# Optimization experiments

Hardware: AMD Instinct MI355X
Metric: run time of the kernel (lower is better)

## Reference

```python
import jax, jax.numpy as jnp
import numpy as np

B, N, F_IN, D_OUT, EMB_DIM = 4, 2048, 64, 128, 16
H1, D1 = 4, D_OUT // 4   # gat1: 4 heads, 32 per head
H2, D2 = 1, D_OUT        # gat2: 1 head, 128
NEG_INF = -1e9
LN_EPS = 1e-3  # keras LayerNormalization default epsilon


def setup_inputs() -> dict:
    key = jax.random.key(0)
    ks = jax.random.split(key, 12)
    def glorot(k, shape):
        lim = np.sqrt(6.0 / (shape[0] + shape[1]))
        return jax.random.uniform(k, shape, jnp.float32, -lim, lim)
    return {
        "x": jax.random.normal(ks[0], (B, N, F_IN), jnp.float32),
        "emb": glorot(ks[1], (N, EMB_DIM)),
        "q1_w": glorot(ks[2], (F_IN, H1 * D1)), "q1_b": jnp.zeros((H1 * D1,), jnp.float32),
        "k1_w": glorot(ks[3], (F_IN, H1 * D1)), "k1_b": jnp.zeros((H1 * D1,), jnp.float32),
        "v1_w": glorot(ks[4], (F_IN, H1 * D1)), "v1_b": jnp.zeros((H1 * D1,), jnp.float32),
        "q2_w": glorot(ks[5], (D_OUT, H2 * D2)), "q2_b": jnp.zeros((H2 * D2,), jnp.float32),
        "k2_w": glorot(ks[6], (D_OUT, H2 * D2)), "k2_b": jnp.zeros((H2 * D2,), jnp.float32),
        "v2_w": glorot(ks[7], (D_OUT, H2 * D2)), "v2_b": jnp.zeros((H2 * D2,), jnp.float32),
        "proj_w": glorot(ks[8], (F_IN, D_OUT)),
        "ln_g": jnp.ones((D_OUT,), jnp.float32),
        "ln_b": jnp.zeros((D_OUT,), jnp.float32),
    }


def _adaptive_adj(emb):
    # tf.math.l2_normalize(axis=-1, epsilon=1e-12)
    sq = jnp.maximum(jnp.sum(emb * emb, axis=-1, keepdims=True), 1e-12)
    n = emb * jax.lax.rsqrt(sq)
    adj = jax.nn.sigmoid(n @ n.T)
    eye = jnp.eye(N, dtype=jnp.float32)
    return adj + eye - adj * eye  # force diag to 1


def _graph_attention(x, adj, qw, qb, kw, kb, vw, vb, heads, d):
    b, n, _ = x.shape
    q = (x @ qw + qb).reshape(b, n, heads, d)
    k = (x @ kw + kb).reshape(b, n, heads, d)
    v = (x @ vw + vb).reshape(b, n, heads, d)
    scores = jnp.einsum('bihd,bjhd->bhij', q, k) / jnp.sqrt(jnp.float32(d))
    scores = jnp.where(adj[None, None] == 0, NEG_INF, scores)
    w = jax.nn.softmax(scores, axis=-1)  # dropout inactive (training=False)
    out = jnp.einsum('bhij,bjhd->bihd', w, v)
    return out.reshape(b, n, heads * d)


def reference(x, emb, q1_w, q1_b, k1_w, k1_b, v1_w, v1_b,
              q2_w, q2_b, k2_w, k2_b, v2_w, v2_b, proj_w, ln_g, ln_b):
    input_projected = x @ proj_w
    adj = _adaptive_adj(emb)
    h = _graph_attention(x, adj, q1_w, q1_b, k1_w, k1_b, v1_w, v1_b, H1, D1)
    h = jax.nn.relu(h)
    h = _graph_attention(h, adj, q2_w, q2_b, k2_w, k2_b, v2_w, v2_b, H2, D2)
    y = h + input_projected
    mu = jnp.mean(y, axis=-1, keepdims=True)
    var = jnp.mean((y - mu) ** 2, axis=-1, keepdims=True)
    return (y - mu) * jax.lax.rsqrt(var + LN_EPS) * ln_g + ln_b
```

## Files before the change

kernel.cpp:

```cpp
#include <hip/hip_runtime.h>
#include <hip/hip_bf16.h>

#define NB 4
#define NN 2048
#define FIN 64
#define DOUT 128

typedef __hip_bfloat16 bf16;
typedef __attribute__((ext_vector_type(8))) short short8;
typedef __attribute__((ext_vector_type(4))) float f32x4;
typedef __attribute__((ext_vector_type(4))) int int4v;

static __device__ __forceinline__ float bf2f(bf16 v) { return __bfloat162float(v); }
static __device__ __forceinline__ bf16  f2bf(float v) { return __float2bfloat16(v); }
static __device__ __forceinline__ unsigned bfbits(float v) {
    bf16 h = __float2bfloat16(v);
    return (unsigned)*reinterpret_cast<unsigned short*>(&h);
}


__global__ __launch_bounds__(256) void k_gemm1(
    const float* __restrict__ x,
    const float* __restrict__ q1w, const float* __restrict__ q1b,
    const float* __restrict__ k1w, const float* __restrict__ k1b,
    const float* __restrict__ v1w, const float* __restrict__ v1b,
    const float* __restrict__ pw,
    bf16* __restrict__ qA, bf16* __restrict__ kA, bf16* __restrict__ vT,
    float* __restrict__ proj)
{
    __shared__ float At[64][65];
    __shared__ float Wt[64][65];
    const int rb = blockIdx.x;
    const int cb = blockIdx.y;
    const int mat = cb >> 1;
    const int c0 = (cb & 1) * 64;
    const float* W    = (mat==0)? q1w : (mat==1)? k1w : (mat==2)? v1w : pw;
    const float* bias = (mat==0)? q1b : (mat==1)? k1b : (mat==2)? v1b : nullptr;
    const int t = threadIdx.x;
    const int row0 = rb * 64;
    for (int e = t; e < 1024; e += 256) {
        int r = e >> 4, c4 = e & 15;
        *(float4*)&At[r][c4*4] = *(const float4*)&x[(size_t)(row0 + r)*FIN + c4*4];
        *(float4*)&Wt[r][c4*4] = *(const float4*)&W[(size_t)r*DOUT + c0 + c4*4];
    }
    __syncthreads();
    const int ty = t >> 4, tx = t & 15;
    float acc[4][4] = {};
    #pragma unroll 8
    for (int k = 0; k < 64; ++k) {
        float av[4], bv[4];
        #pragma unroll
        for (int i = 0; i < 4; ++i) av[i] = At[ty*4+i][k];
        #pragma unroll
        for (int j = 0; j < 4; ++j) bv[j] = Wt[k][tx*4+j];
        #pragma unroll
        for (int i = 0; i < 4; ++i)
            #pragma unroll
            for (int j = 0; j < 4; ++j)
                acc[i][j] = fmaf(av[i], bv[j], acc[i][j]);
    }
    #pragma unroll
    for (int i = 0; i < 4; ++i) {
        int gr = row0 + ty*4 + i;
        int b = gr >> 11, n = gr & 2047;
        #pragma unroll
        for (int j = 0; j < 4; ++j) {
            int gc = c0 + tx*4 + j;
            float v = acc[i][j] + (bias ? bias[gc] : 0.f);
            if (mat == 3) { proj[(size_t)gr*DOUT + gc] = v; continue; }
            int hd = gc >> 5, d32 = gc & 31;
            if (mat == 2) {
                int kt = n >> 6, ks2 = (n >> 5) & 1, q4k = (n >> 3) & 3, jk = n & 7;
                int mt = d32 >> 4, n16d = d32 & 15;
                size_t idx = ((((size_t)(b*4+hd)*32 + kt)*2 + mt)*2 + ks2)*512
                             + (size_t)(q4k*16 + n16d)*8 + jk;
                vT[idx] = f2bf(v);
            } else {
                size_t idx = ((size_t)(b*4+hd)*128 + (n >> 4))*512
                             + (size_t)((d32 >> 3)*16 + (n & 15))*8 + (d32 & 7);
                if (mat == 0) qA[idx] = f2bf(v); else kA[idx] = f2bf(v);
            }
        }
    }
}

__global__ __launch_bounds__(256) void k_gemm2(
    const bf16* __restrict__ h,
    const float* __restrict__ q2w, const float* __restrict__ q2b,
    const float* __restrict__ k2w, const float* __restrict__ k2b,
    const float* __restrict__ v2w, const float* __restrict__ v2b,
    bf16* __restrict__ qA, bf16* __restrict__ kA, bf16* __restrict__ vT)
{
    __shared__ float At[64][65];
    __shared__ float Wt[64][65];
    const int rb = blockIdx.x, cb = blockIdx.y;
    const int mat = cb >> 1, c0 = (cb & 1)*64;
    const float* W    = (mat==0)? q2w : (mat==1)? k2w : v2w;
    const float* bias = (mat==0)? q2b : (mat==1)? k2b : v2b;
    const int t = threadIdx.x, ty = t >> 4, tx = t & 15, row0 = rb*64;
    float acc[4][4] = {};
    for (int kc = 0; kc < 2; ++kc) {
        __syncthreads();
        for (int e = t; e < 512; e += 256) {
            int r = e >> 3, c8 = e & 7;
            short8 hv = *(const short8*)&h[(size_t)(row0+r)*DOUT + kc*64 + c8*8];
            #pragma unroll
            for (int u = 0; u < 8; ++u)
                At[r][c8*8 + u] = __uint_as_float(((unsigned)(unsigned short)hv[u]) << 16);
        }
        for (int e = t; e < 1024; e += 256) {
            int r = e >> 4, c4 = e & 15;
            *(float4*)&Wt[r][c4*4] = *(const float4*)&W[(size_t)(kc*64+r)*DOUT + c0 + c4*4];
        }
        __syncthreads();
        #pragma unroll 8
        for (int k = 0; k < 64; ++k) {
            float av[4], bv[4];
            #pragma unroll
            for (int i = 0; i < 4; ++i) av[i] = At[ty*4+i][k];
            #pragma unroll
            for (int j = 0; j < 4; ++j) bv[j] = Wt[k][tx*4+j];
            #pragma unroll
            for (int i = 0; i < 4; ++i)
                #pragma unroll
                for (int j = 0; j < 4; ++j)
                    acc[i][j] = fmaf(av[i], bv[j], acc[i][j]);
        }
    }
    #pragma unroll
    for (int i = 0; i < 4; ++i) {
        int gr = row0 + ty*4 + i;
        int b = gr >> 11, n = gr & 2047;
        #pragma unroll
        for (int j = 0; j < 4; ++j) {
            int gc = c0 + tx*4 + j;
            float v = acc[i][j] + bias[gc];
            if (mat == 2) {
                int kt = n >> 6, ks2 = (n >> 5) & 1, q4k = (n >> 3) & 3, jk = n & 7;
                int mt = gc >> 4, n16d = gc & 15;
                size_t idx = (((size_t)b*32 + kt)*8 + mt)*1024 + (size_t)ks2*512
                             + (size_t)(q4k*16 + n16d)*8 + jk;
                vT[idx] = f2bf(v);
            } else {
                int ks = gc >> 5, q4 = (gc >> 3) & 3, jj = gc & 7;
                size_t idx = ((size_t)b*128 + (n >> 4))*2048 + (size_t)ks*512
                             + (size_t)(q4*16 + (n & 15))*8 + jj;
                if (mat == 0) qA[idx] = f2bf(v); else kA[idx] = f2bf(v);
            }
        }
    }
}

template<int D, int MODE, int NW, int NQ>
__global__ __launch_bounds__(NW*64, 2) void k_attn_mfma(
    const bf16* __restrict__ qA, const bf16* __restrict__ kA, const bf16* __restrict__ vT,
    const float* __restrict__ proj, const float* __restrict__ lng, const float* __restrict__ lnb,
    bf16* __restrict__ hout, float* __restrict__ fout)
{
    constexpr int NKS = D / 32;
    constexpr int NMT = D / 16;
    constexpr int ITERS = NN / (64 * NW);

    __shared__ float lbuf[NW][NQ*16];
    constexpr int OSW = (MODE == 0) ? (D + 1) : (D + 2);
    __shared__ char oS_raw[(size_t)NW * NQ*16 * OSW * ((MODE == 0) ? 4 : 2)];

    const float scale = (D == 32) ? 0.17677669529663687f : 0.08838834764831843f;

    const unsigned wg  = blockIdx.x + (unsigned)gridDim.x * blockIdx.y;
    const unsigned xcd = wg & 7u;
    const unsigned idx = wg >> 3;
    int qb, bh;
    if constexpr (MODE == 0) {
        bh = (int)((xcd << 1) | (idx >> 5));
        qb = (int)(idx & 31u);
    } else {
        bh = (int)(xcd >> 1);
        qb = (int)(((xcd & 1u) << 5) | idx);
    }

    const int b  = (MODE == 0) ? (bh >> 2) : bh;
    const int hd = (MODE == 0) ? (bh & 3) : 0;
    const int q0 = qb * (16*NQ);
    const int wave = threadIdx.x >> 6, lane = threadIdx.x & 63;
    const int n16 = lane & 15, q4 = lane >> 4;
    const int lane8 = lane * 8;

    const short* qbase, * kbase, * vbase;
    if constexpr (MODE == 0) {
        qbase = (const short*)qA + (size_t)(b*4 + hd)*128*512;
        kbase = (const short*)kA + (size_t)(b*4 + hd)*128*512;
        vbase = (const short*)vT + (size_t)(b*4 + hd)*(32*NMT*2*512);
    } else {
        qbase = (const short*)qA + (size_t)b*128*NKS*512;
        kbase = (const short*)kA + (size_t)b*128*NKS*512;
        vbase = (const short*)vT + (size_t)b*(32*NMT*2*512);
    }

    short8 qf[NQ][NKS];
    #pragma unroll
    for (int qq = 0; qq < NQ; ++qq)
        #pragma unroll
        for (int ks = 0; ks < NKS; ++ks)
            qf[qq][ks] = *(const short8*)(qbase + ((size_t)(qb*NQ + qq)*NKS + ks)*512 + lane8);

    f32x4 acc[NQ][NMT];
    #pragma unroll
    for (int qq = 0; qq < NQ; ++qq)
        #pragma unroll
        for (int mt = 0; mt < NMT; ++mt) acc[qq][mt] = f32x4{0.f, 0.f, 0.f, 0.f};
    float l_lane[NQ];
    #pragma unroll
    for (int qq = 0; qq < NQ; ++qq) l_lane[qq] = 0.f;

    const int srcA = n16 + ((q4 & 1) * 2) * 16;
    const int srcB = srcA + 16;
    const bool selhi = (q4 >= 2);

    for (int kt0 = 0; kt0 < ITERS; ++kt0) {
        const int kt = wave * ITERS + kt0;

        unsigned w0v[NQ][4], w1v[NQ][4];
        #pragma unroll
        for (int mt = 0; mt < 4; ++mt) {
            f32x4 c[NQ];
            #pragma unroll
            for (int qq = 0; qq < NQ; ++qq) c[qq] = f32x4{0.f, 0.f, 0.f, 0.f};
            #pragma unroll
            for (int ks = 0; ks < NKS; ++ks) {
                short8 kf = *(const short8*)(kbase + ((size_t)(kt*4 + mt)*NKS + ks)*512 + lane8);
                #pragma unroll
                for (int qq = 0; qq < NQ; ++qq)
                    c[qq] = __builtin_amdgcn_mfma_f32_16x16x32_bf16(kf, qf[qq][ks], c[qq], 0, 0, 0);
            }
            #pragma unroll
            for (int qq = 0; qq < NQ; ++qq) {
                #pragma unroll
                for (int r = 0; r < 4; ++r) {
                    float p = __expf(c[qq][r] * scale);
                    c[qq][r] = p;
                    l_lane[qq] += p;
                }
                w0v[qq][mt] = bfbits(c[qq][0]) | (bfbits(c[qq][1]) << 16);
                w1v[qq][mt] = bfbits(c[qq][2]) | (bfbits(c[qq][3]) << 16);
            }
        }

        #pragma unroll
        for (int ks2 = 0; ks2 < 2; ++ks2) {
            const int t0 = ks2*2, t1 = ks2*2 + 1;
            short8 pf[NQ];
            #pragma unroll
            for (int qq = 0; qq < NQ; ++qq) {
                int4v pw;
                { unsigned a = __shfl(w0v[qq][t0], srcA), bx = __shfl(w0v[qq][t1], srcA);
                  pw.x = selhi ? (int)bx : (int)a; }
                { unsigned a = __shfl(w1v[qq][t0], srcA), bx = __shfl(w1v[qq][t1], srcA);
                  pw.y = selhi ? (int)bx : (int)a; }
                { unsigned a = __shfl(w0v[qq][t0], srcB), bx = __shfl(w0v[qq][t1], srcB);
                  pw.z = selhi ? (int)bx : (int)a; }
                { unsigned a = __shfl(w1v[qq][t0], srcB), bx = __shfl(w1v[qq][t1], srcB);
                  pw.w = selhi ? (int)bx : (int)a; }
                pf[qq] = __builtin_bit_cast(short8, pw);
            }
            #pragma unroll
            for (int mt = 0; mt < NMT; ++mt) {
                short8 vf = *(const short8*)(vbase + (((size_t)kt*NMT + mt)*2 + ks2)*512 + lane8);
                #pragma unroll
                for (int qq = 0; qq < NQ; ++qq)
                    acc[qq][mt] = __builtin_amdgcn_mfma_f32_16x16x32_bf16(vf, pf[qq], acc[qq][mt], 0, 0, 0);
            }
        }
    }

    #pragma unroll
    for (int qq = 0; qq < NQ; ++qq) {
        l_lane[qq] += __shfl_xor(l_lane[qq], 16);
        l_lane[qq] += __shfl_xor(l_lane[qq], 32);
        if (q4 == 0) lbuf[wave][qq*16 + n16] = l_lane[qq];
    }

    if (MODE == 0) {
        float (&oSf)[NW][NQ*16][D + 1] = *reinterpret_cast<float (*)[NW][NQ*16][D + 1]>(oS_raw);
        #pragma unroll
        for (int qq = 0; qq < NQ; ++qq)
            #pragma unroll
            for (int mt = 0; mt < NMT; ++mt)
                #pragma unroll
                for (int r = 0; r < 4; ++r)
                    oSf[wave][qq*16 + n16][mt*16 + q4*4 + r] = acc[qq][mt][r];
    } else {
        unsigned short (&oSh)[NW][NQ*16][D + 2] =
            *reinterpret_cast<unsigned short (*)[NW][NQ*16][D + 2]>(oS_raw);
        #pragma unroll
        for (int qq = 0; qq < NQ; ++qq)
            #pragma unroll
            for (int mt = 0; mt < NMT; ++mt)
                #pragma unroll
                for (int r = 0; r < 4; ++r)
                    oSh[wave][qq*16 + n16][mt*16 + q4*4 + r] = (unsigned short)bfbits(acc[qq][mt][r]);
    }
    __syncthreads();

    if (MODE == 0) {
        float (&oSf)[NW][NQ*16][D + 1] = *reinterpret_cast<float (*)[NW][NQ*16][D + 1]>(oS_raw);
        if (wave < 4) {
            const int ql = (wave & 3)*4 + (lane >> 4);
            const int d2 = (lane & 15)*2;
            #pragma unroll
            for (int qq = 0; qq < NQ; ++qq) {
                const int row = qq*16 + ql;
                float denom = 0.f, o0 = 0.f, o1 = 0.f;
                #pragma unroll
                for (int s = 0; s < NW; ++s) {
                    denom += lbuf[s][row];
                    o0 += oSf[s][row][d2];
                    o1 += oSf[s][row][d2 + 1];
                }
                float di = 1.f / denom;
                unsigned w = bfbits(fmaxf(o0*di, 0.f)) | (bfbits(fmaxf(o1*di, 0.f)) << 16);
                *(unsigned*)&hout[((size_t)b*NN + q0 + row)*DOUT + hd*32 + d2] = w;
            }
        }
    } else {
        unsigned short (&oSh)[NW][NQ*16][D + 2] =
            *reinterpret_cast<unsigned short (*)[NW][NQ*16][D + 2]>(oS_raw);
        const int ql = wave*2 + (lane >> 5);
        const int il = lane & 31;
        #pragma unroll
        for (int qq = 0; qq < NQ; ++qq) {
            const int row = qq*16 + ql;
            float denom = 0.f;
            #pragma unroll
            for (int s = 0; s < NW; ++s) denom += lbuf[s][row];
            float di = 1.f / denom;
            size_t base = ((size_t)b*NN + q0 + row)*DOUT + il*4;
            float4 pr = *(const float4*)(proj + base);
            float y[4];
            #pragma unroll
            for (int c = 0; c < 4; ++c) {
                float o = 0.f;
                #pragma unroll
                for (int s = 0; s < NW; ++s)
                    o += __uint_as_float(((unsigned)oSh[s][row][il*4 + c]) << 16);
                y[c] = o*di + ((const float*)&pr)[c];
            }
            float ssum = y[0] + y[1] + y[2] + y[3];
            #pragma unroll
            for (int off = 16; off >= 1; off >>= 1) ssum += __shfl_xor(ssum, off);
            float mu = ssum * (1.f/128.f);
            float vs = 0.f;
            #pragma unroll
            for (int c = 0; c < 4; ++c) { float d = y[c] - mu; vs += d*d; }
            #pragma unroll
            for (int off = 16; off >= 1; off >>= 1) vs += __shfl_xor(vs, off);
            float rs = rsqrtf(vs * (1.f/128.f) + 1e-3f);
            float4 g4 = *(const float4*)(lng + il*4);
            float4 b4 = *(const float4*)(lnb + il*4);
            float4 o4;
            #pragma unroll
            for (int c = 0; c < 4; ++c) {
                float o = (y[c] - mu)*rs*((const float*)&g4)[c] + ((const float*)&b4)[c];
                if (!(o == o)) o = 12345.0f;
                ((float*)&o4)[c] = o;
            }
            *(float4*)(fout + base) = o4;
        }
    }
}

extern "C" void kernel_launch(void* const* d_in, const int* in_sizes, int n_in,
                              void* d_out, int out_size, void* d_ws, size_t ws_size,
                              hipStream_t stream)
{
    const float* x   = (const float*)d_in[0];
    const float* q1w = (const float*)d_in[2];
    const float* q1b = (const float*)d_in[3];
    const float* k1w = (const float*)d_in[4];
    const float* k1b = (const float*)d_in[5];
    const float* v1w = (const float*)d_in[6];
    const float* v1b = (const float*)d_in[7];
    const float* q2w = (const float*)d_in[8];
    const float* q2b = (const float*)d_in[9];
    const float* k2w = (const float*)d_in[10];
    const float* k2b = (const float*)d_in[11];
    const float* v2w = (const float*)d_in[12];
    const float* v2b = (const float*)d_in[13];
    const float* pw  = (const float*)d_in[14];
    const float* lng = (const float*)d_in[15];
    const float* lnb = (const float*)d_in[16];

    const size_t SZ = (size_t)NB*NN*DOUT;
    char* wsb = (char*)d_ws;
    bf16*  qA   = (bf16*)(wsb + 0*SZ*2);
    bf16*  kA   = (bf16*)(wsb + 1*SZ*2);
    bf16*  vT   = (bf16*)(wsb + 2*SZ*2);
    float* proj = (float*)(wsb + 3*SZ*2);
    bf16*  h    = (bf16*)(wsb + 3*SZ*2 + SZ*4);

    k_gemm1<<<dim3(128, 8), 256, 0, stream>>>(x, q1w, q1b, k1w, k1b, v1w, v1b, pw,
                                              qA, kA, vT, proj);
    k_attn_mfma<32, 0, 8, 4><<<dim3(32, 16), 512, 0, stream>>>(
        qA, kA, vT, nullptr, nullptr, nullptr, h, nullptr);
    k_gemm2<<<dim3(128, 6), 256, 0, stream>>>(h, q2w, q2b, k2w, k2b, v2w, v2b,
                                              qA, kA, vT);
    k_attn_mfma<128, 1, 8, 2><<<dim3(64, 4), 512, 0, stream>>>(
        qA, kA, vT, proj, lng, lnb, nullptr, (float*)d_out);
}
```

Baseline: 190.2 us.

## Split second attention over key range and merge partials in LayerNorm kernel

```diff
diff --git a/kernel.cpp b/kernel.cpp
--- a/kernel.cpp
+++ b/kernel.cpp
@@ -155,11 +155,12 @@
 __global__ __launch_bounds__(NW*64, 2) void k_attn_mfma(
     const bf16* __restrict__ qA, const bf16* __restrict__ kA, const bf16* __restrict__ vT,
     const float* __restrict__ proj, const float* __restrict__ lng, const float* __restrict__ lnb,
-    bf16* __restrict__ hout, float* __restrict__ fout)
+    bf16* __restrict__ hout, float* __restrict__ fout, float* __restrict__ dout)
 {
     constexpr int NKS = D / 32;
     constexpr int NMT = D / 16;
-    constexpr int ITERS = NN / (64 * NW);
+    constexpr int KSP = (MODE == 1) ? 4 : 1;
+    constexpr int ITERS = NN / (64 * NW * KSP);
 
     __shared__ float lbuf[NW][NQ*16];
     constexpr int OSW = (MODE == 0) ? (D + 1) : (D + 2);
@@ -170,13 +171,14 @@
     const unsigned wg  = blockIdx.x + (unsigned)gridDim.x * blockIdx.y;
     const unsigned xcd = wg & 7u;
     const unsigned idx = wg >> 3;
-    int qb, bh;
+    int qb, bh, ksp = 0;
     if constexpr (MODE == 0) {
         bh = (int)((xcd << 1) | (idx >> 5));
         qb = (int)(idx & 31u);
     } else {
         bh = (int)(xcd >> 1);
-        qb = (int)(((xcd & 1u) << 5) | idx);
+        qb = (int)(((xcd & 1u) << 4) | (idx & 15u));
+        ksp = (int)(idx >> 4);
     }
 
     const int b  = (MODE == 0) ? (bh >> 2) : bh;
@@ -218,57 +220,109 @@
     const bool selhi = (q4 >= 2);
 
     for (int kt0 = 0; kt0 < ITERS; ++kt0) {
-        const int kt = wave * ITERS + kt0;
-
-        unsigned w0v[NQ][4], w1v[NQ][4];
-        #pragma unroll
-        for (int mt = 0; mt < 4; ++mt) {
-            f32x4 c[NQ];
-            #pragma unroll
-            for (int qq = 0; qq < NQ; ++qq) c[qq] = f32x4{0.f, 0.f, 0.f, 0.f};
-            #pragma unroll
-            for (int ks = 0; ks < NKS; ++ks) {
-                short8 kf = *(const short8*)(kbase + ((size_t)(kt*4 + mt)*NKS + ks)*512 + lane8);
-                #pragma unroll
-                for (int qq = 0; qq < NQ; ++qq)
-                    c[qq] = __builtin_amdgcn_mfma_f32_16x16x32_bf16(kf, qf[qq][ks], c[qq], 0, 0, 0);
-            }
-            #pragma unroll
-            for (int qq = 0; qq < NQ; ++qq) {
-                #pragma unroll
-                for (int r = 0; r < 4; ++r) {
-                    float p = __expf(c[qq][r] * scale);
-                    c[qq][r] = p;
-                    l_lane[qq] += p;
-                }
-                w0v[qq][mt] = bfbits(c[qq][0]) | (bfbits(c[qq][1]) << 16);
-                w1v[qq][mt] = bfbits(c[qq][2]) | (bfbits(c[qq][3]) << 16);
-            }
-        }
-
-        #pragma unroll
-        for (int ks2 = 0; ks2 < 2; ++ks2) {
-            const int t0 = ks2*2, t1 = ks2*2 + 1;
-            short8 pf[NQ];
-            #pragma unroll
-            for (int qq = 0; qq < NQ; ++qq) {
-                int4v pw;
-                { unsigned a = __shfl(w0v[qq][t0], srcA), bx = __shfl(w0v[qq][t1], srcA);
-                  pw.x = selhi ? (int)bx : (int)a; }
-                { unsigned a = __shfl(w1v[qq][t0], srcA), bx = __shfl(w1v[qq][t1], srcA);
-                  pw.y = selhi ? (int)bx : (int)a; }
-                { unsigned a = __shfl(w0v[qq][t0], srcB), bx = __shfl(w0v[qq][t1], srcB);
-                  pw.z = selhi ? (int)bx : (int)a; }
-                { unsigned a = __shfl(w1v[qq][t0], srcB), bx = __shfl(w1v[qq][t1], srcB);
-                  pw.w = selhi ? (int)bx : (int)a; }
-                pf[qq] = __builtin_bit_cast(short8, pw);
-            }
-            #pragma unroll
-            for (int mt = 0; mt < NMT; ++mt) {
-                short8 vf = *(const short8*)(vbase + (((size_t)kt*NMT + mt)*2 + ks2)*512 + lane8);
-                #pragma unroll
-                for (int qq = 0; qq < NQ; ++qq)
-                    acc[qq][mt] = __builtin_amdgcn_mfma_f32_16x16x32_bf16(vf, pf[qq], acc[qq][mt], 0, 0, 0);
+        const int kt = ((MODE == 1) ? ksp * (NN/64/KSP) : 0) + wave * ITERS + kt0;
+
+        if constexpr (MODE == 0) {
+            unsigned w0v[NQ][4], w1v[NQ][4];
+            #pragma unroll
+            for (int mt = 0; mt < 4; ++mt) {
+                f32x4 c[NQ];
+                #pragma unroll
+                for (int qq = 0; qq < NQ; ++qq) c[qq] = f32x4{0.f, 0.f, 0.f, 0.f};
+                #pragma unroll
+                for (int ks = 0; ks < NKS; ++ks) {
+                    short8 kf = *(const short8*)(kbase + ((size_t)(kt*4 + mt)*NKS + ks)*512 + lane8);
+                    #pragma unroll
+                    for (int qq = 0; qq < NQ; ++qq)
+                        c[qq] = __builtin_amdgcn_mfma_f32_16x16x32_bf16(kf, qf[qq][ks], c[qq], 0, 0, 0);
+                }
+                #pragma unroll
+                for (int qq = 0; qq < NQ; ++qq) {
+                    #pragma unroll
+                    for (int r = 0; r < 4; ++r) {
+                        float p = __expf(c[qq][r] * scale);
+                        c[qq][r] = p;
+                        l_lane[qq] += p;
+                    }
+                    w0v[qq][mt] = bfbits(c[qq][0]) | (bfbits(c[qq][1]) << 16);
+                    w1v[qq][mt] = bfbits(c[qq][2]) | (bfbits(c[qq][3]) << 16);
+                }
+            }
+            #pragma unroll
+            for (int ks2 = 0; ks2 < 2; ++ks2) {
+                const int t0 = ks2*2, t1 = ks2*2 + 1;
+                short8 pf[NQ];
+                #pragma unroll
+                for (int qq = 0; qq < NQ; ++qq) {
+                    int4v pw;
+                    { unsigned a = __shfl(w0v[qq][t0], srcA), bx = __shfl(w0v[qq][t1], srcA);
+                      pw.x = selhi ? (int)bx : (int)a; }
+                    { unsigned a = __shfl(w1v[qq][t0], srcA), bx = __shfl(w1v[qq][t1], srcA);
+                      pw.y = selhi ? (int)bx : (int)a; }
+                    { unsigned a = __shfl(w0v[qq][t0], srcB), bx = __shfl(w0v[qq][t1], srcB);
+                      pw.z = selhi ? (int)bx : (int)a; }
+                    { unsigned a = __shfl(w1v[qq][t0], srcB), bx = __shfl(w1v[qq][t1], srcB);
+                      pw.w = selhi ? (int)bx : (int)a; }
+                    pf[qq] = __builtin_bit_cast(short8, pw);
+                }
+                #pragma unroll
+                for (int mt = 0; mt < NMT; ++mt) {
+                    short8 vf = *(const short8*)(vbase + (((size_t)kt*NMT + mt)*2 + ks2)*512 + lane8);
+                    #pragma unroll
+                    for (int qq = 0; qq < NQ; ++qq)
+                        acc[qq][mt] = __builtin_amdgcn_mfma_f32_16x16x32_bf16(vf, pf[qq], acc[qq][mt], 0, 0, 0);
+                }
+            }
+        } else {
+            #pragma unroll
+            for (int hh = 0; hh < 2; ++hh) {
+                unsigned w0v[NQ][2], w1v[NQ][2];
+                #pragma unroll
+                for (int m2 = 0; m2 < 2; ++m2) {
+                    const int mt = hh*2 + m2;
+                    f32x4 c[NQ];
+                    #pragma unroll
+                    for (int qq = 0; qq < NQ; ++qq) c[qq] = f32x4{0.f, 0.f, 0.f, 0.f};
+                    #pragma unroll
+                    for (int ks = 0; ks < NKS; ++ks) {
+                        short8 kf = *(const short8*)(kbase + ((size_t)(kt*4 + mt)*NKS + ks)*512 + lane8);
+                        #pragma unroll
+                        for (int qq = 0; qq < NQ; ++qq)
+                            c[qq] = __builtin_amdgcn_mfma_f32_16x16x32_bf16(kf, qf[qq][ks], c[qq], 0, 0, 0);
+                    }
+                    #pragma unroll
+                    for (int qq = 0; qq < NQ; ++qq) {
+                        #pragma unroll
+                        for (int r = 0; r < 4; ++r) {
+                            float p = __expf(c[qq][r] * scale);
+                            c[qq][r] = p;
+                            l_lane[qq] += p;
+                        }
+                        w0v[qq][m2] = bfbits(c[qq][0]) | (bfbits(c[qq][1]) << 16);
+                        w1v[qq][m2] = bfbits(c[qq][2]) | (bfbits(c[qq][3]) << 16);
+                    }
+                }
+                short8 pf[NQ];
+                #pragma unroll
+                for (int qq = 0; qq < NQ; ++qq) {
+                    int4v pw;
+                    { unsigned a = __shfl(w0v[qq][0], srcA), bx = __shfl(w0v[qq][1], srcA);
+                      pw.x = selhi ? (int)bx : (int)a; }
+                    { unsigned a = __shfl(w1v[qq][0], srcA), bx = __shfl(w1v[qq][1], srcA);
+                      pw.y = selhi ? (int)bx : (int)a; }
+                    { unsigned a = __shfl(w0v[qq][0], srcB), bx = __shfl(w0v[qq][1], srcB);
+                      pw.z = selhi ? (int)bx : (int)a; }
+                    { unsigned a = __shfl(w1v[qq][0], srcB), bx = __shfl(w1v[qq][1], srcB);
+                      pw.w = selhi ? (int)bx : (int)a; }
+                    pf[qq] = __builtin_bit_cast(short8, pw);
+                }
+                #pragma unroll
+                for (int mt = 0; mt < NMT; ++mt) {
+                    short8 vf = *(const short8*)(vbase + (((size_t)kt*NMT + mt)*2 + hh)*512 + lane8);
+                    #pragma unroll
+                    for (int qq = 0; qq < NQ; ++qq)
+                        acc[qq][mt] = __builtin_amdgcn_mfma_f32_16x16x32_bf16(vf, pf[qq], acc[qq][mt], 0, 0, 0);
+                }
             }
         }
     }
@@ -325,47 +379,82 @@
     } else {
         unsigned short (&oSh)[NW][NQ*16][D + 2] =
             *reinterpret_cast<unsigned short (*)[NW][NQ*16][D + 2]>(oS_raw);
-        const int ql = wave*2 + (lane >> 5);
-        const int il = lane & 31;
+        const int unit = b*32 + qb;
+        const int ql = wave*4 + (lane >> 4);
+        const int d8 = (lane & 15)*8;
         #pragma unroll
         for (int qq = 0; qq < NQ; ++qq) {
             const int row = qq*16 + ql;
             float denom = 0.f;
             #pragma unroll
             for (int s = 0; s < NW; ++s) denom += lbuf[s][row];
-            float di = 1.f / denom;
-            size_t base = ((size_t)b*NN + q0 + row)*DOUT + il*4;
-            float4 pr = *(const float4*)(proj + base);
-            float y[4];
-            #pragma unroll
-            for (int c = 0; c < 4; ++c) {
-                float o = 0.f;
-                #pragma unroll
-                for (int s = 0; s < NW; ++s)
-                    o += __uint_as_float(((unsigned)oSh[s][row][il*4 + c]) << 16);
-                y[c] = o*di + ((const float*)&pr)[c];
-            }
-            float ssum = y[0] + y[1] + y[2] + y[3];
-            #pragma unroll
-            for (int off = 16; off >= 1; off >>= 1) ssum += __shfl_xor(ssum, off);
-            float mu = ssum * (1.f/128.f);
-            float vs = 0.f;
-            #pragma unroll
-            for (int c = 0; c < 4; ++c) { float d = y[c] - mu; vs += d*d; }
-            #pragma unroll
-            for (int off = 16; off >= 1; off >>= 1) vs += __shfl_xor(vs, off);
-            float rs = rsqrtf(vs * (1.f/128.f) + 1e-3f);
-            float4 g4 = *(const float4*)(lng + il*4);
-            float4 b4 = *(const float4*)(lnb + il*4);
-            float4 o4;
-            #pragma unroll
-            for (int c = 0; c < 4; ++c) {
-                float o = (y[c] - mu)*rs*((const float*)&g4)[c] + ((const float*)&b4)[c];
-                if (!(o == o)) o = 12345.0f;
-                ((float*)&o4)[c] = o;
-            }
-            *(float4*)(fout + base) = o4;
-        }
+            unsigned pk[4];
+            #pragma unroll
+            for (int c2 = 0; c2 < 4; ++c2) {
+                float o0 = 0.f, o1 = 0.f;
+                #pragma unroll
+                for (int s = 0; s < NW; ++s) {
+                    o0 += __uint_as_float(((unsigned)oSh[s][row][d8 + c2*2]) << 16);
+                    o1 += __uint_as_float(((unsigned)oSh[s][row][d8 + c2*2 + 1]) << 16);
+                }
+                pk[c2] = bfbits(o0) | (bfbits(o1) << 16);
+            }
+            int4v pv; pv.x = (int)pk[0]; pv.y = (int)pk[1]; pv.z = (int)pk[2]; pv.w = (int)pk[3];
+            *(int4v*)&hout[(((size_t)ksp*128 + unit)*64 + row)*128 + d8] = pv;
+            if (d8 == 0) dout[((size_t)ksp*128 + unit)*64 + row] = denom;
+        }
+    }
+}
+
+__global__ __launch_bounds__(512) void k_merge_ln(
+    const bf16* __restrict__ P, const float* __restrict__ Dn,
+    const float* __restrict__ proj, const float* __restrict__ lng, const float* __restrict__ lnb,
+    float* __restrict__ fout)
+{
+    const int u = blockIdx.x;
+    const int b = u >> 5, qb = u & 31;
+    const int q0 = qb * 64;
+    const int wave = threadIdx.x >> 6, lane = threadIdx.x & 63;
+    const int ql = wave*2 + (lane >> 5);
+    const int il = lane & 31;
+    #pragma unroll
+    for (int qq = 0; qq < 4; ++qq) {
+        const int row = qq*16 + ql;
+        float denom = 0.f;
+        #pragma unroll
+        for (int s = 0; s < 4; ++s) denom += Dn[((size_t)s*128 + u)*64 + row];
+        float di = 1.f / denom;
+        size_t base = ((size_t)b*NN + q0 + row)*DOUT + il*4;
+        float4 pr = *(const float4*)(proj + base);
+        float y[4];
+        #pragma unroll
+        for (int c = 0; c < 4; ++c) {
+            float o = 0.f;
+            #pragma unroll
+            for (int s = 0; s < 4; ++s)
+                o += bf2f(P[(((size_t)s*128 + u)*64 + row)*128 + il*4 + c]);
+            y[c] = o*di + ((const float*)&pr)[c];
+        }
+        float ssum = y[0] + y[1] + y[2] + y[3];
+        #pragma unroll
+        for (int off = 16; off >= 1; off >>= 1) ssum += __shfl_xor(ssum, off);
+        float mu = ssum * (1.f/128.f);
+        float vs = 0.f;
+        #pragma unroll
+        for (int c = 0; c < 4; ++c) { float d = y[c] - mu; vs += d*d; }
+        #pragma unroll
+        for (int off = 16; off >= 1; off >>= 1) vs += __shfl_xor(vs, off);
+        float rs = rsqrtf(vs * (1.f/128.f) + 1e-3f);
+        float4 g4 = *(const float4*)(lng + il*4);
+        float4 b4 = *(const float4*)(lnb + il*4);
+        float4 o4;
+        #pragma unroll
+        for (int c = 0; c < 4; ++c) {
+            float o = (y[c] - mu)*rs*((const float*)&g4)[c] + ((const float*)&b4)[c];
+            if (!(o == o)) o = 12345.0f;
+            ((float*)&o4)[c] = o;
+        }
+        *(float4*)(fout + base) = o4;
     }
 }
 
@@ -397,13 +486,16 @@
     bf16*  vT   = (bf16*)(wsb + 2*SZ*2);
     float* proj = (float*)(wsb + 3*SZ*2);
     bf16*  h    = (bf16*)(wsb + 3*SZ*2 + SZ*4);
+    bf16*  P    = (bf16*)(wsb + (size_t)12*1024*1024);
+    float* Dn   = (float*)(wsb + (size_t)20*1024*1024);
 
     k_gemm1<<<dim3(128, 8), 256, 0, stream>>>(x, q1w, q1b, k1w, k1b, v1w, v1b, pw,
                                               qA, kA, vT, proj);
     k_attn_mfma<32, 0, 8, 4><<<dim3(32, 16), 512, 0, stream>>>(
-        qA, kA, vT, nullptr, nullptr, nullptr, h, nullptr);
+        qA, kA, vT, nullptr, nullptr, nullptr, h, nullptr, nullptr);
     k_gemm2<<<dim3(128, 6), 256, 0, stream>>>(h, q2w, q2b, k2w, k2b, v2w, v2b,
                                               qA, kA, vT);
-    k_attn_mfma<128, 1, 8, 2><<<dim3(64, 4), 512, 0, stream>>>(
-        qA, kA, vT, proj, lng, lnb, nullptr, (float*)d_out);
+    k_attn_mfma<128, 1, 4, 4><<<dim3(64, 8), 256, 0, stream>>>(
+        qA, kA, vT, nullptr, nullptr, nullptr, P, nullptr, Dn);
+    k_merge_ln<<<dim3(128), 512, 0, stream>>>(P, Dn, proj, lng, lnb, (float*)d_out);
 }
```

After: 206.3 us. 1.08x slower.

## Assign attention work items by actual XCC id via atomic claiming

Applied to the files above, without the earlier changes.

```diff
diff --git a/kernel.cpp b/kernel.cpp
--- a/kernel.cpp
+++ b/kernel.cpp
@@ -17,6 +17,7 @@
     bf16 h = __float2bfloat16(v);
     return (unsigned)*reinterpret_cast<unsigned short*>(&h);
 }
+
 
 
 __global__ __launch_bounds__(256) void k_gemm1(
@@ -26,8 +27,11 @@
     const float* __restrict__ v1w, const float* __restrict__ v1b,
     const float* __restrict__ pw,
     bf16* __restrict__ qA, bf16* __restrict__ kA, bf16* __restrict__ vT,
-    float* __restrict__ proj)
+    float* __restrict__ proj, int* __restrict__ ctrl)
 {
+    if (blockIdx.x == 0 && blockIdx.y == 0) {
+        for (int e = threadIdx.x; e < 784; e += 256) ctrl[e] = 0;
+    }
     __shared__ float At[64][65];
     __shared__ float Wt[64][65];
     const int rb = blockIdx.x;
@@ -155,32 +159,48 @@
 __global__ __launch_bounds__(NW*64, 2) void k_attn_mfma(
     const bf16* __restrict__ qA, const bf16* __restrict__ kA, const bf16* __restrict__ vT,
     const float* __restrict__ proj, const float* __restrict__ lng, const float* __restrict__ lnb,
-    bf16* __restrict__ hout, float* __restrict__ fout)
+    bf16* __restrict__ hout, float* __restrict__ fout, int* __restrict__ ctrl)
 {
     constexpr int NKS = D / 32;
     constexpr int NMT = D / 16;
     constexpr int ITERS = NN / (64 * NW);
+    constexpr int NITEMS = (MODE == 0) ? 512 : 256;
 
     __shared__ float lbuf[NW][NQ*16];
+    __shared__ int s_item;
     constexpr int OSW = (MODE == 0) ? (D + 1) : (D + 2);
     __shared__ char oS_raw[(size_t)NW * NQ*16 * OSW * ((MODE == 0) ? 4 : 2)];
 
     const float scale = (D == 32) ? 0.17677669529663687f : 0.08838834764831843f;
 
-    const unsigned wg  = blockIdx.x + (unsigned)gridDim.x * blockIdx.y;
-    const unsigned xcd = wg & 7u;
-    const unsigned idx = wg >> 3;
-    int qb, bh;
+    if (threadIdx.x == 0) {
+        unsigned xcc;
+        asm volatile("s_getreg_b32 %0, hwreg(HW_REG_XCC_ID)" : "=s"(xcc));
+        xcc &= 7u;
+        int* claim = ctrl + ((MODE == 0) ? 0 : 512);
+        int* ctr   = ctrl + ((MODE == 0) ? 768 : 776);
+        int start;
+        if constexpr (MODE == 0) start = (int)xcc * 64;
+        else                     start = (int)(xcc >> 1) * 64 + (int)(xcc & 1) * 32;
+        int seq = atomicAdd(&ctr[xcc], 1);
+        int item = -1;
+        for (int a = 0; a < NITEMS; ++a) {
+            int it = (start + seq + a) & (NITEMS - 1);
+            if (atomicCAS(&claim[it], 0, 1) == 0) { item = it; break; }
+        }
+        s_item = item;
+    }
+    __syncthreads();
+    const int item = s_item;
+
+    int b, hd, qb;
     if constexpr (MODE == 0) {
-        bh = (int)((xcd << 1) | (idx >> 5));
-        qb = (int)(idx & 31u);
+        int bh = item >> 5; qb = item & 31;
+        b = bh >> 2; hd = bh & 3;
     } else {
-        bh = (int)(xcd >> 1);
-        qb = (int)(((xcd & 1u) << 5) | idx);
-    }
-
-    const int b  = (MODE == 0) ? (bh >> 2) : bh;
-    const int hd = (MODE == 0) ? (bh & 3) : 0;
+        b = item >> 6; qb = item & 63; hd = 0;
+    }
+
     const int q0 = qb * (16*NQ);
     const int wave = threadIdx.x >> 6, lane = threadIdx.x & 63;
     const int n16 = lane & 15, q4 = lane >> 4;
@@ -245,7 +265,6 @@
                 w1v[qq][mt] = bfbits(c[qq][2]) | (bfbits(c[qq][3]) << 16);
             }
         }
-
         #pragma unroll
         for (int ks2 = 0; ks2 < 2; ++ks2) {
             const int t0 = ks2*2, t1 = ks2*2 + 1;
@@ -397,13 +416,14 @@
     bf16*  vT   = (bf16*)(wsb + 2*SZ*2);
     float* proj = (float*)(wsb + 3*SZ*2);
     bf16*  h    = (bf16*)(wsb + 3*SZ*2 + SZ*4);
+    int*   ctrl = (int*)(wsb + (size_t)12*1024*1024);
 
     k_gemm1<<<dim3(128, 8), 256, 0, stream>>>(x, q1w, q1b, k1w, k1b, v1w, v1b, pw,
-                                              qA, kA, vT, proj);
+                                              qA, kA, vT, proj, ctrl);
     k_attn_mfma<32, 0, 8, 4><<<dim3(32, 16), 512, 0, stream>>>(
-        qA, kA, vT, nullptr, nullptr, nullptr, h, nullptr);
+        qA, kA, vT, nullptr, nullptr, nullptr, h, nullptr, ctrl);
     k_gemm2<<<dim3(128, 6), 256, 0, stream>>>(h, q2w, q2b, k2w, k2b, v2w, v2b,
                                               qA, kA, vT);
     k_attn_mfma<128, 1, 8, 2><<<dim3(64, 4), 512, 0, stream>>>(
-        qA, kA, vT, proj, lng, lnb, nullptr, (float*)d_out);
+        qA, kA, vT, proj, lng, lnb, nullptr, (float*)d_out, ctrl);
 }
```

Result: slower. 199.2 us (+4.7%).
